# Optimization experiments

Measured on AMD Instinct MI355X. Metric: run time of the kernel, lower is better.

Reference implementation:

```python
import jax, jax.numpy as jnp
import numpy as np

B, N, E, G, V = 32, 128, 2048, 1024, 10000
D_IN, HID, MID = 20, 1024, 128
EPS = 1e-5


def _bn(x, gamma, beta, axis):
    # train-mode BatchNorm: biased variance over `axis`
    mu = jnp.mean(x, axis=axis, keepdims=True)
    var = jnp.mean((x - mu) ** 2, axis=axis, keepdims=True)
    return gamma * (x - mu) / jnp.sqrt(var + EPS) + beta


def _gin_mean(h, src, dst):
    # DGL GINConv(apply_func=None, 'mean', eps=0): h + mean over in-neighbors
    b, n, d = h.shape
    offs = (jnp.arange(b, dtype=src.dtype) * n)[:, None]
    sf = (src + offs).reshape(-1)
    df = (dst + offs).reshape(-1)
    hf = h.reshape(b * n, d)
    agg = jax.ops.segment_sum(hf[sf], df, num_segments=b * n)
    deg = jax.ops.segment_sum(jnp.ones(sf.shape, h.dtype), df, num_segments=b * n)
    mean = agg / jnp.maximum(deg, 1.0)[:, None]
    return h + mean.reshape(b, n, d)


def setup_inputs() -> dict:
    key = jax.random.key(0)
    ks = jax.random.split(key, 12)
    inp = {
        'h': jax.random.normal(ks[0], (B, N, D_IN), jnp.float32),
        'edge_src': jax.random.randint(ks[1], (B, E), 0, N),
        'edge_dst': jax.random.randint(ks[2], (B, E), 0, N),
        'gPos': jax.random.randint(ks[3], (B, G), 0, V),
        'allDBGEmb': jax.random.normal(ks[4], (V, HID), jnp.float32) * 0.1,
        'W_init': jax.random.normal(ks[5], (D_IN, HID), jnp.float32) / np.sqrt(D_IN),
        'b_init': jnp.zeros((HID,), jnp.float32),
        'gamma1': jnp.ones((HID,), jnp.float32),
        'beta1': jnp.zeros((HID,), jnp.float32),
        'gamma2': jnp.ones((HID,), jnp.float32),
        'beta2': jnp.zeros((HID,), jnp.float32),
        'W_fc': jax.random.normal(ks[6], (2 * HID, MID), jnp.float32) / np.sqrt(2 * HID),
        'b_fc': jnp.zeros((MID,), jnp.float32),
        'gamma_bn': jnp.ones((MID,), jnp.float32),
        'beta_bn': jnp.zeros((MID,), jnp.float32),
        'W_fc2': jax.random.normal(ks[7], (MID, 1), jnp.float32) / np.sqrt(MID),
        'b_fc2': jnp.zeros((1,), jnp.float32),
    }
    return inp


def reference(h, edge_src, edge_dst, gPos, allDBGEmb, W_init, b_init,
              gamma1, beta1, gamma2, beta2, W_fc, b_fc, gamma_bn, beta_bn,
              W_fc2, b_fc2):
    # per-query-graph GNN encoder
    h2 = h @ W_init + b_init                       # [B,N,HID]
    h2 = jax.nn.relu(_bn(_gin_mean(h2, edge_src, edge_dst), gamma1, beta1, axis=1))
    h2 = jax.nn.relu(_bn(_gin_mean(h2, edge_src, edge_dst), gamma2, beta2, axis=1))
    qemb = jnp.mean(h2, axis=1)                    # [B,HID] (dgl.mean_nodes)
    # pairwise scoring head
    gEmb = allDBGEmb[gPos]                         # [B,G,HID]
    q_rep = jnp.broadcast_to(qemb[:, None, :], gEmb.shape)
    H = jnp.concatenate([q_rep, gEmb], axis=-1)    # [B,G,2*HID]
    H2 = jax.nn.relu(_bn(H @ W_fc + b_fc, gamma_bn, beta_bn, axis=1))  # BN over G
    probs = jax.nn.sigmoid(H2 @ W_fc2 + b_fc2)[..., 0]  # [B,G]
    return probs
```

## Files before the change

kernel.cpp:

```cpp
#include <hip/hip_runtime.h>
#include <hip/hip_bf16.h>

#define BB 32
#define GG 1024
#define VV 10000
#define KHID 1024
#define MM 128
#define NCHUNK 625

typedef __attribute__((ext_vector_type(8))) short short8;
typedef __attribute__((ext_vector_type(4))) float f32x4;

__device__ __forceinline__ unsigned int pk2(float lo, float hi) {
    __hip_bfloat162 h = __float22bfloat162_rn(make_float2(lo, hi));
    union { __hip_bfloat162 h; unsigned int u; } cv; cv.h = h;
    return cv.u;
}

__device__ __forceinline__ float bfu(unsigned short u) {
    union { unsigned int u; float f; } v; v.u = (unsigned int)u << 16;
    return v.f;
}

__device__ __forceinline__ void lds_barrier() {
    asm volatile("s_waitcnt lgkmcnt(0)" ::: "memory");
    __builtin_amdgcn_s_barrier();
    asm volatile("" ::: "memory");
}

__global__ __launch_bounds__(512, 2) void k_gemm(const float* __restrict__ A,
                                                 const float* __restrict__ Wfc,
                                                 unsigned short* __restrict__ T) {
    const int tid = threadIdx.x;
    const int w = tid >> 6, lane = tid & 63;
    const int r16 = lane & 15, g = lane >> 4;
    const int kbase = w * 128;
    const int chunk = blockIdx.x;

    float4 a[8];
    {
        const float* Ap = A + (size_t)(chunk * 16 + r16) * KHID + kbase + g * 8;
#pragma unroll
        for (int kt = 0; kt < 4; ++kt) {
            a[2 * kt]     = *(const float4*)(Ap + kt * 32);
            a[2 * kt + 1] = *(const float4*)(Ap + kt * 32 + 4);
        }
    }

    const float* Wg = Wfc + (size_t)KHID * MM;
    short8 breg[4][8];
#pragma unroll
    for (int kt = 0; kt < 4; ++kt)
#pragma unroll
        for (int t = 0; t < 8; ++t) {
            const float* wp = Wg + (size_t)(kbase + kt * 32 + g * 8) * MM + t * 16 + r16;
            unsigned int* bu = (unsigned int*)&breg[kt][t];
            bu[0] = pk2(wp[0 * MM], wp[1 * MM]);
            bu[1] = pk2(wp[2 * MM], wp[3 * MM]);
            bu[2] = pk2(wp[4 * MM], wp[5 * MM]);
            bu[3] = pk2(wp[6 * MM], wp[7 * MM]);
        }

    f32x4 acc[8];
#pragma unroll
    for (int t = 0; t < 8; ++t) acc[t] = (f32x4){0.f, 0.f, 0.f, 0.f};
#pragma unroll
    for (int kt = 0; kt < 4; ++kt) {
        short8 af;
        unsigned int* au = (unsigned int*)&af;
        au[0] = pk2(a[2 * kt].x, a[2 * kt].y);
        au[1] = pk2(a[2 * kt].z, a[2 * kt].w);
        au[2] = pk2(a[2 * kt + 1].x, a[2 * kt + 1].y);
        au[3] = pk2(a[2 * kt + 1].z, a[2 * kt + 1].w);
#pragma unroll
        for (int t = 0; t < 8; ++t)
            acc[t] = __builtin_amdgcn_mfma_f32_16x16x32_bf16(af, breg[kt][t], acc[t],
                                                             0, 0, 0);
    }

    __shared__ float red[8][16][128];
#pragma unroll
    for (int t = 0; t < 8; ++t)
#pragma unroll
        for (int r = 0; r < 4; ++r)
            red[w][g * 4 + r][t * 16 + r16] = acc[t][r];
    lds_barrier();

    const int orow = tid >> 5, c4 = (tid & 31) * 4;
    float4 s = *(const float4*)&red[0][orow][c4];
#pragma unroll
    for (int sl = 1; sl < 8; ++sl) {
        float4 p = *(const float4*)&red[sl][orow][c4];
        s.x += p.x; s.y += p.y; s.z += p.z; s.w += p.w;
    }
    *(uint2*)&T[(size_t)(chunk * 16 + orow) * MM + c4] =
        make_uint2(pk2(s.x, s.y), pk2(s.z, s.w));
}

__global__ __launch_bounds__(256) void k_stats(const unsigned short* __restrict__ T,
                                               const int* __restrict__ gPos,
                                               float* __restrict__ ps1,
                                               float* __restrict__ ps2) {
    const int b = blockIdx.y, c = blockIdx.x;
    const int tid = threadIdx.x;

    __shared__ int posl[32];
    __shared__ float r1[4][128], r2[4][128];

    if (tid < 32) posl[tid] = gPos[b * GG + c * 32 + tid];
    __syncthreads();

    const int m = tid & 63, q = tid >> 6;
    unsigned int uu[8];
#pragma unroll
    for (int i = 0; i < 8; ++i)
        uu[i] = *(const unsigned int*)&T[(size_t)posl[q * 8 + i] * MM + m * 2];

    float s1a = 0.f, s1b = 0.f, s2a = 0.f, s2b = 0.f;
#pragma unroll
    for (int i = 0; i < 8; ++i) {
        float t0 = bfu((unsigned short)(uu[i] & 0xFFFFu));
        float t1 = bfu((unsigned short)(uu[i] >> 16));
        s1a += t0; s2a += t0 * t0;
        s1b += t1; s2b += t1 * t1;
    }
    r1[q][m * 2] = s1a; r1[q][m * 2 + 1] = s1b;
    r2[q][m * 2] = s2a; r2[q][m * 2 + 1] = s2b;
    __syncthreads();
    if (tid < 128) {
        ps1[((size_t)b * 32 + c) * MM + tid] = r1[0][tid] + r1[1][tid] + r1[2][tid] + r1[3][tid];
        ps2[((size_t)b * 32 + c) * MM + tid] = r2[0][tid] + r2[1][tid] + r2[2][tid] + r2[3][tid];
    }
}

__global__ __launch_bounds__(256) void k_final(const unsigned short* __restrict__ T,
                                               const int* __restrict__ gPos,
                                               const float* __restrict__ ps1,
                                               const float* __restrict__ ps2,
                                               const float* __restrict__ gamma,
                                               const float* __restrict__ beta,
                                               const float* __restrict__ W2,
                                               const float* __restrict__ b2,
                                               float* __restrict__ out) {
    const int b = blockIdx.y, gc = blockIdx.x;
    const int tid = threadIdx.x;

    __shared__ float ssc[128], ssh[128];
    __shared__ int posl[32];
    if (tid < 32) posl[tid] = gPos[b * GG + gc * 32 + tid];
    if (tid >= 128) {
        int mcol = tid - 128;
        float S1 = 0.f, S2 = 0.f;
#pragma unroll
        for (int cc = 0; cc < 32; ++cc) {
            S1 += ps1[((size_t)b * 32 + cc) * MM + mcol];
            S2 += ps2[((size_t)b * 32 + cc) * MM + mcol];
        }
        float mean = S1 * (1.f / 1024.f);
        float var  = S2 * (1.f / 1024.f) - mean * mean;
        float rstd = rsqrtf(var + 1e-5f);
        float sc = gamma[mcol] * rstd;
        ssc[mcol] = sc;
        ssh[mcol] = beta[mcol] - sc * mean;
    }
    __syncthreads();

    const int wave = tid >> 6, lane = tid & 63;
    const int m0 = lane * 2, m1 = lane * 2 + 1;
    const float sc0 = ssc[m0], sh0 = ssh[m0], w20 = W2[m0];
    const float sc1 = ssc[m1], sh1 = ssh[m1], w21 = W2[m1];
    const float bias = b2[0];

    unsigned int uu[8];
#pragma unroll
    for (int i = 0; i < 8; ++i)
        uu[i] = *(const unsigned int*)&T[(size_t)posl[wave * 8 + i] * MM + m0];

#pragma unroll
    for (int i = 0; i < 8; ++i) {
        float t0 = bfu((unsigned short)(uu[i] & 0xFFFFu));
        float t1 = bfu((unsigned short)(uu[i] >> 16));
        float val = fmaxf(sc0 * t0 + sh0, 0.f) * w20 + fmaxf(sc1 * t1 + sh1, 0.f) * w21;
#pragma unroll
        for (int off = 32; off; off >>= 1) val += __shfl_xor(val, off, 64);
        if (lane == 0)
            out[b * GG + gc * 32 + wave * 8 + i] = 1.f / (1.f + __expf(-(val + bias)));
    }
}

extern "C" void kernel_launch(void* const* d_in, const int* in_sizes, int n_in,
                              void* d_out, int out_size, void* d_ws, size_t ws_size,
                              hipStream_t stream) {
    const int*   gPos  = (const int*)d_in[3];
    const float* A     = (const float*)d_in[4];
    const float* Wfc   = (const float*)d_in[11];
    const float* gamma = (const float*)d_in[13];
    const float* beta  = (const float*)d_in[14];
    const float* W2    = (const float*)d_in[15];
    const float* b2    = (const float*)d_in[16];
    float* out = (float*)d_out;

    char* ws = (char*)d_ws;
    unsigned short* T = (unsigned short*)ws;
    float* ps1 = (float*)(ws + (4 << 20));
    float* ps2 = (float*)(ws + (8 << 20));

    hipLaunchKernelGGL(k_gemm, dim3(NCHUNK), dim3(512), 0, stream, A, Wfc, T);
    hipLaunchKernelGGL(k_stats, dim3(32, BB), dim3(256), 0, stream, T, gPos, ps1, ps2);
    hipLaunchKernelGGL(k_final, dim3(32, BB), dim3(256), 0, stream, T, gPos, ps1, ps2,
                       gamma, beta, W2, b2, out);
}
```

Before: 40.55 us.

## Make GEMM kernel persistent over chunks with double-buffered A prefetch

The embedding-table GEMM kernel now launches 256 blocks, each handling two or three 16-row chunks, instead of one block per chunk (625). The converted bf16 W fragments are loaded once per block and reused across its chunks. A-tile loads for the next chunks are issued ahead of the MFMA work, so global latency overlaps with compute. This adds a second LDS barrier per chunk and keeps more registers live, which could limit occupancy, and the work split across blocks is uneven.

```diff
diff --git a/kernel.cpp b/kernel.cpp
--- a/kernel.cpp
+++ b/kernel.cpp
@@ -7,6 +7,7 @@
 #define KHID 1024
 #define MM 128
 #define NCHUNK 625
+#define GEMM_GRID 256
 
 typedef __attribute__((ext_vector_type(8))) short short8;
 typedef __attribute__((ext_vector_type(4))) float f32x4;
@@ -27,6 +28,46 @@
     __builtin_amdgcn_s_barrier();
     asm volatile("" ::: "memory");
 }
+
+#define LOAD_A(areg, cc)                                                          \
+    {                                                                             \
+        const float* Ap_ = A + (size_t)((cc) * 16 + r16) * KHID + kbase + g * 8;  \
+        _Pragma("unroll") for (int kt = 0; kt < 4; ++kt) {                        \
+            areg[2 * kt]     = *(const float4*)(Ap_ + kt * 32);                   \
+            areg[2 * kt + 1] = *(const float4*)(Ap_ + kt * 32 + 4);               \
+        }                                                                         \
+    }
+
+#define PROCESS(areg, cc, refill)                                                 \
+    {                                                                             \
+        f32x4 acc[8];                                                             \
+        _Pragma("unroll") for (int t = 0; t < 8; ++t)                             \
+            acc[t] = (f32x4){0.f, 0.f, 0.f, 0.f};                                 \
+        _Pragma("unroll") for (int kt = 0; kt < 4; ++kt) {                        \
+            short8 af;                                                            \
+            unsigned int* au = (unsigned int*)&af;                                \
+            au[0] = pk2(areg[2 * kt].x, areg[2 * kt].y);                          \
+            au[1] = pk2(areg[2 * kt].z, areg[2 * kt].w);                          \
+            au[2] = pk2(areg[2 * kt + 1].x, areg[2 * kt + 1].y);                  \
+            au[3] = pk2(areg[2 * kt + 1].z, areg[2 * kt + 1].w);                  \
+            _Pragma("unroll") for (int t = 0; t < 8; ++t)                         \
+                acc[t] = __builtin_amdgcn_mfma_f32_16x16x32_bf16(                 \
+                    af, breg[kt][t], acc[t], 0, 0, 0);                            \
+        }                                                                         \
+        if (refill) LOAD_A(areg, (cc) + 2 * GEMM_GRID);                           \
+        _Pragma("unroll") for (int t = 0; t < 8; ++t)                             \
+            _Pragma("unroll") for (int r = 0; r < 4; ++r)                         \
+                red[w][g * 4 + r][t * 16 + r16] = acc[t][r];                      \
+        lds_barrier();                                                            \
+        float4 s = *(const float4*)&red[0][orow][c4];                             \
+        _Pragma("unroll") for (int sl = 1; sl < 8; ++sl) {                        \
+            float4 p = *(const float4*)&red[sl][orow][c4];                        \
+            s.x += p.x; s.y += p.y; s.z += p.z; s.w += p.w;                       \
+        }                                                                         \
+        *(uint2*)&T[(size_t)((cc) * 16 + orow) * MM + c4] =                       \
+            make_uint2(pk2(s.x, s.y), pk2(s.z, s.w));                             \
+        lds_barrier();                                                            \
+    }
 
 __global__ __launch_bounds__(512, 2) void k_gemm(const float* __restrict__ A,
                                                  const float* __restrict__ Wfc,
@@ -35,17 +76,11 @@
     const int w = tid >> 6, lane = tid & 63;
     const int r16 = lane & 15, g = lane >> 4;
     const int kbase = w * 128;
-    const int chunk = blockIdx.x;
-
-    float4 a[8];
-    {
-        const float* Ap = A + (size_t)(chunk * 16 + r16) * KHID + kbase + g * 8;
-#pragma unroll
-        for (int kt = 0; kt < 4; ++kt) {
-            a[2 * kt]     = *(const float4*)(Ap + kt * 32);
-            a[2 * kt + 1] = *(const float4*)(Ap + kt * 32 + 4);
-        }
-    }
+    const int c0 = blockIdx.x;
+
+    float4 aA[8], aB[8];
+    LOAD_A(aA, c0);
+    LOAD_A(aB, c0 + GEMM_GRID);
 
     const float* Wg = Wfc + (size_t)KHID * MM;
     short8 breg[4][8];
@@ -61,40 +96,22 @@
             bu[3] = pk2(wp[6 * MM], wp[7 * MM]);
         }
 
-    f32x4 acc[8];
-#pragma unroll
-    for (int t = 0; t < 8; ++t) acc[t] = (f32x4){0.f, 0.f, 0.f, 0.f};
-#pragma unroll
-    for (int kt = 0; kt < 4; ++kt) {
-        short8 af;
-        unsigned int* au = (unsigned int*)&af;
-        au[0] = pk2(a[2 * kt].x, a[2 * kt].y);
-        au[1] = pk2(a[2 * kt].z, a[2 * kt].w);
-        au[2] = pk2(a[2 * kt + 1].x, a[2 * kt + 1].y);
-        au[3] = pk2(a[2 * kt + 1].z, a[2 * kt + 1].w);
+#pragma unroll
+    for (int kt = 0; kt < 4; ++kt)
 #pragma unroll
         for (int t = 0; t < 8; ++t)
-            acc[t] = __builtin_amdgcn_mfma_f32_16x16x32_bf16(af, breg[kt][t], acc[t],
-                                                             0, 0, 0);
-    }
+            asm volatile("" : "+v"(breg[kt][t]));
 
     __shared__ float red[8][16][128];
-#pragma unroll
-    for (int t = 0; t < 8; ++t)
-#pragma unroll
-        for (int r = 0; r < 4; ++r)
-            red[w][g * 4 + r][t * 16 + r16] = acc[t][r];
-    lds_barrier();
-
     const int orow = tid >> 5, c4 = (tid & 31) * 4;
-    float4 s = *(const float4*)&red[0][orow][c4];
-#pragma unroll
-    for (int sl = 1; sl < 8; ++sl) {
-        float4 p = *(const float4*)&red[sl][orow][c4];
-        s.x += p.x; s.y += p.y; s.z += p.z; s.w += p.w;
-    }
-    *(uint2*)&T[(size_t)(chunk * 16 + orow) * MM + c4] =
-        make_uint2(pk2(s.x, s.y), pk2(s.z, s.w));
+
+    const bool has3 = (c0 + 2 * GEMM_GRID) < NCHUNK;
+
+    PROCESS(aA, c0, has3);
+    PROCESS(aB, c0 + GEMM_GRID, false);
+    if (has3) {
+        PROCESS(aA, c0 + 2 * GEMM_GRID, false);
+    }
 }
 
 __global__ __launch_bounds__(256) void k_stats(const unsigned short* __restrict__ T,
@@ -205,7 +222,7 @@
     float* ps1 = (float*)(ws + (4 << 20));
     float* ps2 = (float*)(ws + (8 << 20));
 
-    hipLaunchKernelGGL(k_gemm, dim3(NCHUNK), dim3(512), 0, stream, A, Wfc, T);
+    hipLaunchKernelGGL(k_gemm, dim3(GEMM_GRID), dim3(512), 0, stream, A, Wfc, T);
     hipLaunchKernelGGL(k_stats, dim3(32, BB), dim3(256), 0, stream, T, gPos, ps1, ps2);
     hipLaunchKernelGGL(k_final, dim3(32, BB), dim3(256), 0, stream, T, gPos, ps1, ps2,
                        gamma, beta, W2, b2, out);
```

Result: faster. 33.38 us (-17.7%).
